# Performance work log

Hardware: AMD Instinct MI355X
Metric: run time of the kernel (lower is better)

## Reference

```python
import jax, jax.numpy as jnp
import numpy as np

K = 4            # number of expert kernels
TEMPERATURE = 30.0  # T_max, initial temperature
KS = 3
PAD = 1
STRIDE = 1


def setup_inputs() -> dict:
    key = jax.random.key(0)
    k1, k2, k3, k4, k5 = jax.random.split(key, 5)
    b, c_in, c_out, f, t, ctx = 32, 256, 256, 64, 64, 256
    x = jax.random.normal(k1, (b, c_in, f, t), dtype=jnp.float32)
    g = jax.random.normal(k2, (b, ctx), dtype=jnp.float32)
    # expert kernels: (k, out, in//groups, ks, ks), kaiming-normal-ish init
    fan_in = c_in * KS * KS
    weight = jax.random.normal(k3, (K, c_out, c_in, KS, KS), dtype=jnp.float32) * jnp.sqrt(2.0 / fan_in)
    # attention Dense: ctx -> k * att_groups (att_groups = 1)
    dense_w = jax.random.normal(k4, (ctx, K), dtype=jnp.float32) * jnp.sqrt(1.0 / ctx)
    dense_b = jnp.zeros((K,), dtype=jnp.float32)
    return {"x": x, "g": g, "weight": weight, "dense_w": dense_w, "dense_b": dense_b}


def reference(x, g, weight, dense_w, dense_b):
    b, c, f, t = x.shape
    k, c_out, c_in_pg, ks, _ = weight.shape
    # attention over k expert kernels, per batch element (att_groups = 1)
    logits = g @ dense_w + dense_b                      # (b, k)
    attention = jax.nn.softmax(logits / TEMPERATURE, axis=-1)
    # per-sample mixed kernel: (b, out, in, ks, ks)
    agg_w = jnp.einsum('bk,koihw->boihw', attention, weight)
    agg_w = agg_w.reshape(b * c_out, c_in_pg, ks, ks)
    # batched per-sample conv via feature_group_count = groups * b (groups = 1)
    xg = x.reshape(1, b * c, f, t)
    out = jax.lax.conv_general_dilated(
        xg, agg_w,
        window_strides=(STRIDE, STRIDE),
        padding=((PAD, PAD), (PAD, PAD)),
        lhs_dilation=(1, 1), rhs_dilation=(1, 1),
        dimension_numbers=('NCHW', 'OIHW', 'NCHW'),
        feature_group_count=b,
    )
    return out.reshape(b, c_out, out.shape[-2], out.shape[-1])
```

## Files before the change

kernel.cpp:

```cpp
#include <hip/hip_runtime.h>
#include <hip/hip_bf16.h>
#include <stdint.h>

#define BATCH 32
#define CIN   256
#define COUT  256
#define FH    64
#define FW    64
#define NK    4
#define CTX   256
#define TEMP  30.0f

typedef __attribute__((ext_vector_type(8))) short bf16x8;
typedef __attribute__((ext_vector_type(4))) float f32x4;

__device__ __forceinline__ unsigned short f2bf(float f) {
    union { float f; uint32_t u; } a; a.f = f;
    uint32_t r = a.u + 0x7fffu + ((a.u >> 16) & 1u);
    return (unsigned short)(r >> 16);
}

#define WMIX_OFF  1024
#define WMIX_BYTES (32u * 9u * 8u * 4u * 256u * 16u)
#define XP_OFF    (WMIX_OFF + WMIX_BYTES)

__global__ __launch_bounds__(256, 2) void mix_kernel(
        const float* __restrict__ weight,
        const float* __restrict__ g,
        const float* __restrict__ dw,
        const float* __restrict__ db,
        uint32_t* __restrict__ wmix) {
    __shared__ __align__(16) short S[2 * 8 * 2308];
    __shared__ float logit_s[8];
    __shared__ float att_s[8];

    const int t   = threadIdx.x;
    const int cog = blockIdx.x;
    const int bg  = blockIdx.y;
    const int co0 = cog * 8;
    const int b0  = bg * 2;
    const size_t EST = (size_t)COUT * CIN * 9;

    {
        const int p  = t >> 5;
        const int i0 = t & 31;
        const int nb = p >> 2, k = p & 3;
        const float* gp = g + (size_t)(b0 + nb) * CTX;
        float part = 0.f;
#pragma unroll
        for (int j = 0; j < 8; ++j) {
            const int i = i0 + j * 32;
            part += gp[i] * dw[i * NK + k];
        }
#pragma unroll
        for (int m = 1; m <= 16; m <<= 1) part += __shfl_xor(part, m);
        if (i0 == 0) logit_s[p] = part + db[k];
    }
    __syncthreads();
    if (t < 8) {
        const int nb = t >> 2;
        const float l0 = logit_s[nb * 4 + 0] * (1.f / TEMP);
        const float l1 = logit_s[nb * 4 + 1] * (1.f / TEMP);
        const float l2 = logit_s[nb * 4 + 2] * (1.f / TEMP);
        const float l3 = logit_s[nb * 4 + 3] * (1.f / TEMP);
        const float m  = fmaxf(fmaxf(l0, l1), fmaxf(l2, l3));
        const float e0 = expf(l0 - m), e1 = expf(l1 - m);
        const float e2 = expf(l2 - m), e3 = expf(l3 - m);
        const float s  = e0 + e1 + e2 + e3;
        const int   k  = t & 3;
        const float e  = (k == 0) ? e0 : (k == 1) ? e1 : (k == 2) ? e2 : e3;
        att_s[t] = e / s;
    }
    __syncthreads();

    float a[2][4];
#pragma unroll
    for (int nb = 0; nb < 2; ++nb)
#pragma unroll
        for (int k = 0; k < 4; ++k)
            a[nb][k] = att_s[nb * 4 + k];

    const int co_l  = t >> 5;
    const int inner = t & 31;
    const float* wbase = weight + (size_t)(co0 + co_l) * 2304;

#pragma unroll 2
    for (int i = 0; i < 18; ++i) {
        const int e4 = inner + 32 * i;
        float4 w[4];
#pragma unroll
        for (int k = 0; k < 4; ++k)
            w[k] = *(const float4*)(wbase + k * EST + (size_t)e4 * 4);
#pragma unroll
        for (int nb = 0; nb < 2; ++nb) {
            float mx = a[nb][0] * w[0].x + a[nb][1] * w[1].x + a[nb][2] * w[2].x + a[nb][3] * w[3].x;
            float my = a[nb][0] * w[0].y + a[nb][1] * w[1].y + a[nb][2] * w[2].y + a[nb][3] * w[3].y;
            float mz = a[nb][0] * w[0].z + a[nb][1] * w[1].z + a[nb][2] * w[2].z + a[nb][3] * w[3].z;
            float mw = a[nb][0] * w[0].w + a[nb][1] * w[1].w + a[nb][2] * w[2].w + a[nb][3] * w[3].w;
            uint32_t lo = (uint32_t)f2bf(mx) | ((uint32_t)f2bf(my) << 16);
            uint32_t hi = (uint32_t)f2bf(mz) | ((uint32_t)f2bf(mw) << 16);
            uint2* d = (uint2*)(S + ((nb * 8 + co_l) * 2308 + e4 * 4));
            *d = make_uint2(lo, hi);
        }
    }
    __syncthreads();

    const int co_w = t & 7;
    const int slot = t >> 3;
#pragma unroll 2
    for (int j = 0; j < 18; ++j) {
        const int GG  = j * 32 + slot;
        const int b_l = (GG >= 288) ? 1 : 0;
        const int rem = GG - b_l * 288;
        const int tap = rem >> 5;
        const int ch  = (rem >> 2) & 7;
        const int q   = rem & 3;
        const short* sp = S + (b_l * 8 + co_w) * 2308;
        const int ebase = (ch * 32 + q * 8) * 9 + tap;
        uint32_t d[4];
#pragma unroll
        for (int rp = 0; rp < 4; ++rp) {
            uint32_t lo = (uint16_t)sp[ebase + (2 * rp) * 9];
            uint32_t hi = (uint16_t)sp[ebase + (2 * rp + 1) * 9];
            d[rp] = lo | (hi << 16);
        }
        uint32_t* dst = wmix +
            ((((size_t)((b0 + b_l) * 9 + tap) * 8 + ch) * 4 + q) * 256 + co0 + co_w) * 4;
        *(uint4*)dst = make_uint4(d[0], d[1], d[2], d[3]);
    }
}

__global__ __launch_bounds__(256) void xpad_kernel(const float* __restrict__ x,
                                                   uint32_t* __restrict__ xp) {
    __shared__ uint32_t P[6 * 1088];
    const int t  = threadIdx.x;
    const int yg = blockIdx.x;
    const int ch = blockIdx.y;
    const int b  = blockIdx.z;

    for (int i = t; i < 6 * 1088; i += 256) P[i] = 0;
    __syncthreads();

    const int ci_l = t >> 3;
    const int col0 = (t & 7) * 8;
    const int q = ci_l >> 3, r = ci_l & 7;
    unsigned short* Ps = (unsigned short*)P;

#pragma unroll
    for (int yy = 0; yy < 6; ++yy) {
        const int y = yg * 6 + yy;
        if (y >= 1 && y <= 64) {
            const float* xr = x + (((size_t)(b * 256 + ch * 32 + ci_l) * 64) + (y - 1)) * 64 + col0;
            float4 v0 = *(const float4*)xr;
            float4 v1 = *(const float4*)(xr + 4);
            unsigned short bf[8];
            bf[0] = f2bf(v0.x); bf[1] = f2bf(v0.y); bf[2] = f2bf(v0.z); bf[3] = f2bf(v0.w);
            bf[4] = f2bf(v1.x); bf[5] = f2bf(v1.y); bf[6] = f2bf(v1.z); bf[7] = f2bf(v1.w);
#pragma unroll
            for (int j = 0; j < 8; ++j)
                Ps[yy * 2176 + (q * 68 + (col0 + j + 1)) * 8 + r] = bf[j];
        }
    }
    __syncthreads();

    const int qo = t >> 6, l = t & 63;
#pragma unroll
    for (int yy = 0; yy < 6; ++yy) {
        const int y = yg * 6 + yy;
        uint32_t* base = xp + (((((size_t)(b * 8 + ch) * 4 + qo) * 66) + y) * 68) * 4;
#pragma unroll
        for (int i = 0; i < 4; ++i)
            base[l + i * 64] = P[yy * 1088 + qo * 272 + l + i * 64];
        if (l < 16) base[l + 256] = P[yy * 1088 + qo * 272 + l + 256];
    }
}

__global__ __launch_bounds__(256, 2) void conv_mfma(
        const char* __restrict__ xp,
        const char* __restrict__ wmix,
        float* __restrict__ out) {
    __shared__ __align__(16) char As[2][3 * 4 * 2064];
    __shared__ __align__(16) char Bs[2][4 * 2192];

    const int tid  = threadIdx.x;
    const int lane = tid & 63;
    const int wv   = tid >> 6;
    const int wm   = wv & 1;
    const int wn   = wv >> 1;
    const int l4   = lane >> 4;
    const int m16  = lane & 15;

    const int bx  = blockIdx.x;
    const int wid = (bx & 7) * 256 + (bx >> 3);
    const int ptile = wid & 31;
    const int coT   = (wid >> 5) & 1;
    const int b     = wid >> 6;
    const int y0    = ptile * 2;

    const char* wmix_b = wmix + (size_t)b * 9 * 8 * 4 * 256 * 16;
    const char* xp_b   = xp + (size_t)b * 8 * 4 * 66 * 68 * 16;

    f32x4 acc[4][4];
#pragma unroll
    for (int i = 0; i < 4; ++i)
#pragma unroll
        for (int j = 0; j < 4; ++j)
            acc[i][j] = (f32x4){0.f, 0.f, 0.f, 0.f};

    const int aLane = l4 * 2064 + wm * 1024 + m16 * 16;
    const int bLane = l4 * 2192 + wn * 1088 + m16 * 16;

    auto stage = [&](char* Asb, char* Bsb, int p) {
        const int ch = p / 3, dy = p - ch * 3;
#pragma unroll
        for (int i = 0; i < 6; ++i) {
            const int s  = wv + i * 4;
            const int dx = s >> 3;
            const int q  = (s >> 1) & 3;
            const int h  = s & 1;
            const char* gsrc = wmix_b
                + ((size_t)((dy * 3 + dx) * 8 + ch) * 4 + q) * 4096
                + (coT * 128 + h * 64 + lane) * 16;
            char* ldst = Asb + dx * 8256 + q * 2064 + (h * 64 + lane) * 16;
            __builtin_amdgcn_global_load_lds(
                (const __attribute__((address_space(1))) void*)gsrc,
                (__attribute__((address_space(3))) void*)ldst, 16, 0, 0);
        }
        const int yb = y0 + dy;
        const char* gsrc = xp_b
            + (((size_t)ch * 4 + wv) * 66 + yb) * 1088 + lane * 16;
        char* ldst = Bsb + wv * 2192 + lane * 16;
        __builtin_amdgcn_global_load_lds(
            (const __attribute__((address_space(1))) void*)gsrc,
            (__attribute__((address_space(3))) void*)ldst, 16, 0, 0);
        __builtin_amdgcn_global_load_lds(
            (const __attribute__((address_space(1))) void*)(gsrc + 1024),
            (__attribute__((address_space(3))) void*)(ldst + 1024), 16, 0, 0);
        if (lane < 8)
            __builtin_amdgcn_global_load_lds(
                (const __attribute__((address_space(1))) void*)(gsrc + 2048),
                (__attribute__((address_space(3))) void*)(ldst + 2048), 16, 0, 0);
    };

    stage(As[0], Bs[0], 0);
    __syncthreads();

#pragma unroll 1
    for (int p = 0; p < 24; ++p) {
        const int cur = p & 1;
        if (p < 23) stage(As[cur ^ 1], Bs[cur ^ 1], p + 1);

        const char* Asc = As[cur];
        const char* Bsc = Bs[cur];
#pragma unroll
        for (int dx = 0; dx < 3; ++dx) {
            bf16x8 a[4], bb[4];
#pragma unroll
            for (int sm = 0; sm < 4; ++sm)
                a[sm] = *(const bf16x8*)(Asc + dx * 8256 + aLane + sm * 256);
#pragma unroll
            for (int sn = 0; sn < 4; ++sn)
                bb[sn] = *(const bf16x8*)(Bsc + bLane + dx * 16 + sn * 256);
            __builtin_amdgcn_s_setprio(1);
#pragma unroll
            for (int sm = 0; sm < 4; ++sm)
#pragma unroll
                for (int sn = 0; sn < 4; ++sn)
                    acc[sm][sn] = __builtin_amdgcn_mfma_f32_16x16x32_bf16(
                        a[sm], bb[sn], acc[sm][sn], 0, 0, 0);
            __builtin_amdgcn_s_setprio(0);
        }
        __syncthreads();
    }

    const int y = y0 + wn;
#pragma unroll
    for (int sm = 0; sm < 4; ++sm) {
#pragma unroll
        for (int sn = 0; sn < 4; ++sn) {
#pragma unroll
            for (int r = 0; r < 4; ++r) {
                const int co = coT * 128 + wm * 64 + sm * 16 + l4 * 4 + r;
                const int xx = sn * 16 + m16;
                out[(((size_t)b * COUT + co) * FH + y) * FW + xx] = acc[sm][sn][r];
            }
        }
    }
}

extern "C" void kernel_launch(void* const* d_in, const int* in_sizes, int n_in,
                              void* d_out, int out_size, void* d_ws, size_t ws_size,
                              hipStream_t stream) {
    const float* x       = (const float*)d_in[0];
    const float* g       = (const float*)d_in[1];
    const float* weight  = (const float*)d_in[2];
    const float* dense_w = (const float*)d_in[3];
    const float* dense_b = (const float*)d_in[4];
    float* out = (float*)d_out;

    uint32_t* wmix = (uint32_t*)((char*)d_ws + WMIX_OFF);
    uint32_t* xp   = (uint32_t*)((char*)d_ws + XP_OFF);

    mix_kernel<<<dim3(32, 16), 256, 0, stream>>>(weight, g, dense_w, dense_b, wmix);
    xpad_kernel<<<dim3(11, 8, BATCH), 256, 0, stream>>>(x, xp);
    conv_mfma<<<2048, 256, 0, stream>>>((const char*)xp, (const char*)wmix, out);
}
```

Measured before the change: 417.6 us.

## Merge prep kernels and read conv operands directly from global without LDS staging

Folds the weight-mixing and input-padding kernels into one launch whose blocks branch on block index, which saves a kernel launch and its serialization. The conv kernel drops its double-buffered LDS staging and loads MFMA operands straight from global memory into registers, relying on L1/L2 for reuse, and raises the occupancy hint to three blocks per CU. This removes LDS traffic and barriers, but each wave now fetches its operands separately and the global load latency is no longer hidden by explicit prefetch.

```diff
diff --git a/kernel.cpp b/kernel.cpp
--- a/kernel.cpp
+++ b/kernel.cpp
@@ -24,164 +24,166 @@
 #define WMIX_BYTES (32u * 9u * 8u * 4u * 256u * 16u)
 #define XP_OFF    (WMIX_OFF + WMIX_BYTES)
 
-__global__ __launch_bounds__(256, 2) void mix_kernel(
+__global__ __launch_bounds__(256, 2) void prep_kernel(
         const float* __restrict__ weight,
         const float* __restrict__ g,
         const float* __restrict__ dw,
         const float* __restrict__ db,
-        uint32_t* __restrict__ wmix) {
-    __shared__ __align__(16) short S[2 * 8 * 2308];
+        uint32_t* __restrict__ wmix,
+        const float* __restrict__ x,
+        uint32_t* __restrict__ xp) {
+    __shared__ __align__(16) char LDSU[73856];
     __shared__ float logit_s[8];
     __shared__ float att_s[8];
 
+    const int bid = blockIdx.x;
     const int t   = threadIdx.x;
-    const int cog = blockIdx.x;
-    const int bg  = blockIdx.y;
-    const int co0 = cog * 8;
-    const int b0  = bg * 2;
-    const size_t EST = (size_t)COUT * CIN * 9;
-
-    {
-        const int p  = t >> 5;
-        const int i0 = t & 31;
-        const int nb = p >> 2, k = p & 3;
-        const float* gp = g + (size_t)(b0 + nb) * CTX;
-        float part = 0.f;
-#pragma unroll
-        for (int j = 0; j < 8; ++j) {
-            const int i = i0 + j * 32;
-            part += gp[i] * dw[i * NK + k];
-        }
-#pragma unroll
-        for (int m = 1; m <= 16; m <<= 1) part += __shfl_xor(part, m);
-        if (i0 == 0) logit_s[p] = part + db[k];
+
+    if (bid < 512) {
+        short* S = (short*)LDSU;
+        const int cog = bid & 31;
+        const int bg  = bid >> 5;
+        const int co0 = cog * 8;
+        const int b0  = bg * 2;
+        const size_t EST = (size_t)COUT * CIN * 9;
+
+        {
+            const int p  = t >> 5;
+            const int i0 = t & 31;
+            const int nb = p >> 2, k = p & 3;
+            const float* gp = g + (size_t)(b0 + nb) * CTX;
+            float part = 0.f;
+#pragma unroll
+            for (int j = 0; j < 8; ++j) {
+                const int i = i0 + j * 32;
+                part += gp[i] * dw[i * NK + k];
+            }
+#pragma unroll
+            for (int m = 1; m <= 16; m <<= 1) part += __shfl_xor(part, m);
+            if (i0 == 0) logit_s[p] = part + db[k];
+        }
+        __syncthreads();
+        if (t < 8) {
+            const int nb = t >> 2;
+            const float l0 = logit_s[nb * 4 + 0] * (1.f / TEMP);
+            const float l1 = logit_s[nb * 4 + 1] * (1.f / TEMP);
+            const float l2 = logit_s[nb * 4 + 2] * (1.f / TEMP);
+            const float l3 = logit_s[nb * 4 + 3] * (1.f / TEMP);
+            const float m  = fmaxf(fmaxf(l0, l1), fmaxf(l2, l3));
+            const float e0 = expf(l0 - m), e1 = expf(l1 - m);
+            const float e2 = expf(l2 - m), e3 = expf(l3 - m);
+            const float s  = e0 + e1 + e2 + e3;
+            const int   k  = t & 3;
+            const float e  = (k == 0) ? e0 : (k == 1) ? e1 : (k == 2) ? e2 : e3;
+            att_s[t] = e / s;
+        }
+        __syncthreads();
+
+        float a[2][4];
+#pragma unroll
+        for (int nb = 0; nb < 2; ++nb)
+#pragma unroll
+            for (int k = 0; k < 4; ++k)
+                a[nb][k] = att_s[nb * 4 + k];
+
+        const int co_l  = t >> 5;
+        const int inner = t & 31;
+        const float* wbase = weight + (size_t)(co0 + co_l) * 2304;
+
+#pragma unroll 2
+        for (int i = 0; i < 18; ++i) {
+            const int e4 = inner + 32 * i;
+            float4 w[4];
+#pragma unroll
+            for (int k = 0; k < 4; ++k)
+                w[k] = *(const float4*)(wbase + k * EST + (size_t)e4 * 4);
+#pragma unroll
+            for (int nb = 0; nb < 2; ++nb) {
+                float mx = a[nb][0] * w[0].x + a[nb][1] * w[1].x + a[nb][2] * w[2].x + a[nb][3] * w[3].x;
+                float my = a[nb][0] * w[0].y + a[nb][1] * w[1].y + a[nb][2] * w[2].y + a[nb][3] * w[3].y;
+                float mz = a[nb][0] * w[0].z + a[nb][1] * w[1].z + a[nb][2] * w[2].z + a[nb][3] * w[3].z;
+                float mw = a[nb][0] * w[0].w + a[nb][1] * w[1].w + a[nb][2] * w[2].w + a[nb][3] * w[3].w;
+                uint32_t lo = (uint32_t)f2bf(mx) | ((uint32_t)f2bf(my) << 16);
+                uint32_t hi = (uint32_t)f2bf(mz) | ((uint32_t)f2bf(mw) << 16);
+                uint2* d = (uint2*)(S + ((nb * 8 + co_l) * 2308 + e4 * 4));
+                *d = make_uint2(lo, hi);
+            }
+        }
+        __syncthreads();
+
+        const int co_w = t & 7;
+        const int slot = t >> 3;
+#pragma unroll 2
+        for (int j = 0; j < 18; ++j) {
+            const int GG  = j * 32 + slot;
+            const int b_l = (GG >= 288) ? 1 : 0;
+            const int rem = GG - b_l * 288;
+            const int tap = rem >> 5;
+            const int ch  = (rem >> 2) & 7;
+            const int q   = rem & 3;
+            const short* sp = S + (b_l * 8 + co_w) * 2308;
+            const int ebase = (ch * 32 + q * 8) * 9 + tap;
+            uint32_t d[4];
+#pragma unroll
+            for (int rp = 0; rp < 4; ++rp) {
+                uint32_t lo = (uint16_t)sp[ebase + (2 * rp) * 9];
+                uint32_t hi = (uint16_t)sp[ebase + (2 * rp + 1) * 9];
+                d[rp] = lo | (hi << 16);
+            }
+            uint32_t* dst = wmix +
+                ((((size_t)((b0 + b_l) * 9 + tap) * 8 + ch) * 4 + q) * 256 + co0 + co_w) * 4;
+            *(uint4*)dst = make_uint4(d[0], d[1], d[2], d[3]);
+        }
+    } else {
+        uint32_t* P = (uint32_t*)LDSU;
+        const int idx = bid - 512;
+        const int yg  = idx % 11;
+        const int rem = idx / 11;
+        const int ch  = rem & 7;
+        const int b   = rem >> 3;
+
+        for (int i = t; i < 6 * 1088; i += 256) P[i] = 0;
+        __syncthreads();
+
+        const int ci_l = t >> 3;
+        const int col0 = (t & 7) * 8;
+        const int q = ci_l >> 3, r = ci_l & 7;
+        unsigned short* Ps = (unsigned short*)P;
+
+#pragma unroll
+        for (int yy = 0; yy < 6; ++yy) {
+            const int y = yg * 6 + yy;
+            if (y >= 1 && y <= 64) {
+                const float* xr = x + (((size_t)(b * 256 + ch * 32 + ci_l) * 64) + (y - 1)) * 64 + col0;
+                float4 v0 = *(const float4*)xr;
+                float4 v1 = *(const float4*)(xr + 4);
+                unsigned short bf[8];
+                bf[0] = f2bf(v0.x); bf[1] = f2bf(v0.y); bf[2] = f2bf(v0.z); bf[3] = f2bf(v0.w);
+                bf[4] = f2bf(v1.x); bf[5] = f2bf(v1.y); bf[6] = f2bf(v1.z); bf[7] = f2bf(v1.w);
+#pragma unroll
+                for (int j = 0; j < 8; ++j)
+                    Ps[yy * 2176 + (q * 68 + (col0 + j + 1)) * 8 + r] = bf[j];
+            }
+        }
+        __syncthreads();
+
+        const int qo = t >> 6, l = t & 63;
+#pragma unroll
+        for (int yy = 0; yy < 6; ++yy) {
+            const int y = yg * 6 + yy;
+            uint32_t* base = xp + (((((size_t)(b * 8 + ch) * 4 + qo) * 66) + y) * 68) * 4;
+#pragma unroll
+            for (int i = 0; i < 4; ++i)
+                base[l + i * 64] = P[yy * 1088 + qo * 272 + l + i * 64];
+            if (l < 16) base[l + 256] = P[yy * 1088 + qo * 272 + l + 256];
+        }
     }
-    __syncthreads();
-    if (t < 8) {
-        const int nb = t >> 2;
-        const float l0 = logit_s[nb * 4 + 0] * (1.f / TEMP);
-        const float l1 = logit_s[nb * 4 + 1] * (1.f / TEMP);
-        const float l2 = logit_s[nb * 4 + 2] * (1.f / TEMP);
-        const float l3 = logit_s[nb * 4 + 3] * (1.f / TEMP);
-        const float m  = fmaxf(fmaxf(l0, l1), fmaxf(l2, l3));
-        const float e0 = expf(l0 - m), e1 = expf(l1 - m);
-        const float e2 = expf(l2 - m), e3 = expf(l3 - m);
-        const float s  = e0 + e1 + e2 + e3;
-        const int   k  = t & 3;
-        const float e  = (k == 0) ? e0 : (k == 1) ? e1 : (k == 2) ? e2 : e3;
-        att_s[t] = e / s;
-    }
-    __syncthreads();
-
-    float a[2][4];
-#pragma unroll
-    for (int nb = 0; nb < 2; ++nb)
-#pragma unroll
-        for (int k = 0; k < 4; ++k)
-            a[nb][k] = att_s[nb * 4 + k];
-
-    const int co_l  = t >> 5;
-    const int inner = t & 31;
-    const float* wbase = weight + (size_t)(co0 + co_l) * 2304;
-
-#pragma unroll 2
-    for (int i = 0; i < 18; ++i) {
-        const int e4 = inner + 32 * i;
-        float4 w[4];
-#pragma unroll
-        for (int k = 0; k < 4; ++k)
-            w[k] = *(const float4*)(wbase + k * EST + (size_t)e4 * 4);
-#pragma unroll
-        for (int nb = 0; nb < 2; ++nb) {
-            float mx = a[nb][0] * w[0].x + a[nb][1] * w[1].x + a[nb][2] * w[2].x + a[nb][3] * w[3].x;
-            float my = a[nb][0] * w[0].y + a[nb][1] * w[1].y + a[nb][2] * w[2].y + a[nb][3] * w[3].y;
-            float mz = a[nb][0] * w[0].z + a[nb][1] * w[1].z + a[nb][2] * w[2].z + a[nb][3] * w[3].z;
-            float mw = a[nb][0] * w[0].w + a[nb][1] * w[1].w + a[nb][2] * w[2].w + a[nb][3] * w[3].w;
-            uint32_t lo = (uint32_t)f2bf(mx) | ((uint32_t)f2bf(my) << 16);
-            uint32_t hi = (uint32_t)f2bf(mz) | ((uint32_t)f2bf(mw) << 16);
-            uint2* d = (uint2*)(S + ((nb * 8 + co_l) * 2308 + e4 * 4));
-            *d = make_uint2(lo, hi);
-        }
-    }
-    __syncthreads();
-
-    const int co_w = t & 7;
-    const int slot = t >> 3;
-#pragma unroll 2
-    for (int j = 0; j < 18; ++j) {
-        const int GG  = j * 32 + slot;
-        const int b_l = (GG >= 288) ? 1 : 0;
-        const int rem = GG - b_l * 288;
-        const int tap = rem >> 5;
-        const int ch  = (rem >> 2) & 7;
-        const int q   = rem & 3;
-        const short* sp = S + (b_l * 8 + co_w) * 2308;
-        const int ebase = (ch * 32 + q * 8) * 9 + tap;
-        uint32_t d[4];
-#pragma unroll
-        for (int rp = 0; rp < 4; ++rp) {
-            uint32_t lo = (uint16_t)sp[ebase + (2 * rp) * 9];
-            uint32_t hi = (uint16_t)sp[ebase + (2 * rp + 1) * 9];
-            d[rp] = lo | (hi << 16);
-        }
-        uint32_t* dst = wmix +
-            ((((size_t)((b0 + b_l) * 9 + tap) * 8 + ch) * 4 + q) * 256 + co0 + co_w) * 4;
-        *(uint4*)dst = make_uint4(d[0], d[1], d[2], d[3]);
-    }
-}
-
-__global__ __launch_bounds__(256) void xpad_kernel(const float* __restrict__ x,
-                                                   uint32_t* __restrict__ xp) {
-    __shared__ uint32_t P[6 * 1088];
-    const int t  = threadIdx.x;
-    const int yg = blockIdx.x;
-    const int ch = blockIdx.y;
-    const int b  = blockIdx.z;
-
-    for (int i = t; i < 6 * 1088; i += 256) P[i] = 0;
-    __syncthreads();
-
-    const int ci_l = t >> 3;
-    const int col0 = (t & 7) * 8;
-    const int q = ci_l >> 3, r = ci_l & 7;
-    unsigned short* Ps = (unsigned short*)P;
-
-#pragma unroll
-    for (int yy = 0; yy < 6; ++yy) {
-        const int y = yg * 6 + yy;
-        if (y >= 1 && y <= 64) {
-            const float* xr = x + (((size_t)(b * 256 + ch * 32 + ci_l) * 64) + (y - 1)) * 64 + col0;
-            float4 v0 = *(const float4*)xr;
-            float4 v1 = *(const float4*)(xr + 4);
-            unsigned short bf[8];
-            bf[0] = f2bf(v0.x); bf[1] = f2bf(v0.y); bf[2] = f2bf(v0.z); bf[3] = f2bf(v0.w);
-            bf[4] = f2bf(v1.x); bf[5] = f2bf(v1.y); bf[6] = f2bf(v1.z); bf[7] = f2bf(v1.w);
-#pragma unroll
-            for (int j = 0; j < 8; ++j)
-                Ps[yy * 2176 + (q * 68 + (col0 + j + 1)) * 8 + r] = bf[j];
-        }
-    }
-    __syncthreads();
-
-    const int qo = t >> 6, l = t & 63;
-#pragma unroll
-    for (int yy = 0; yy < 6; ++yy) {
-        const int y = yg * 6 + yy;
-        uint32_t* base = xp + (((((size_t)(b * 8 + ch) * 4 + qo) * 66) + y) * 68) * 4;
-#pragma unroll
-        for (int i = 0; i < 4; ++i)
-            base[l + i * 64] = P[yy * 1088 + qo * 272 + l + i * 64];
-        if (l < 16) base[l + 256] = P[yy * 1088 + qo * 272 + l + 256];
-    }
-}
-
-__global__ __launch_bounds__(256, 2) void conv_mfma(
+}
+
+__global__ __launch_bounds__(256, 3) void conv_mfma(
         const char* __restrict__ xp,
         const char* __restrict__ wmix,
         float* __restrict__ out) {
-    __shared__ __align__(16) char As[2][3 * 4 * 2064];
-    __shared__ __align__(16) char Bs[2][4 * 2192];
-
     const int tid  = threadIdx.x;
     const int lane = tid & 63;
     const int wv   = tid >> 6;
@@ -207,73 +209,38 @@
         for (int j = 0; j < 4; ++j)
             acc[i][j] = (f32x4){0.f, 0.f, 0.f, 0.f};
 
-    const int aLane = l4 * 2064 + wm * 1024 + m16 * 16;
-    const int bLane = l4 * 2192 + wn * 1088 + m16 * 16;
-
-    auto stage = [&](char* Asb, char* Bsb, int p) {
-        const int ch = p / 3, dy = p - ch * 3;
-#pragma unroll
-        for (int i = 0; i < 6; ++i) {
-            const int s  = wv + i * 4;
-            const int dx = s >> 3;
-            const int q  = (s >> 1) & 3;
-            const int h  = s & 1;
-            const char* gsrc = wmix_b
-                + ((size_t)((dy * 3 + dx) * 8 + ch) * 4 + q) * 4096
-                + (coT * 128 + h * 64 + lane) * 16;
-            char* ldst = Asb + dx * 8256 + q * 2064 + (h * 64 + lane) * 16;
-            __builtin_amdgcn_global_load_lds(
-                (const __attribute__((address_space(1))) void*)gsrc,
-                (__attribute__((address_space(3))) void*)ldst, 16, 0, 0);
-        }
-        const int yb = y0 + dy;
-        const char* gsrc = xp_b
-            + (((size_t)ch * 4 + wv) * 66 + yb) * 1088 + lane * 16;
-        char* ldst = Bsb + wv * 2192 + lane * 16;
-        __builtin_amdgcn_global_load_lds(
-            (const __attribute__((address_space(1))) void*)gsrc,
-            (__attribute__((address_space(3))) void*)ldst, 16, 0, 0);
-        __builtin_amdgcn_global_load_lds(
-            (const __attribute__((address_space(1))) void*)(gsrc + 1024),
-            (__attribute__((address_space(3))) void*)(ldst + 1024), 16, 0, 0);
-        if (lane < 8)
-            __builtin_amdgcn_global_load_lds(
-                (const __attribute__((address_space(1))) void*)(gsrc + 2048),
-                (__attribute__((address_space(3))) void*)(ldst + 2048), 16, 0, 0);
-    };
-
-    stage(As[0], Bs[0], 0);
-    __syncthreads();
+    const char* Abase = wmix_b + (size_t)l4 * 4096
+                      + (size_t)(coT * 128 + wm * 64 + m16) * 16;
+    const int yout = y0 + wn;
 
 #pragma unroll 1
-    for (int p = 0; p < 24; ++p) {
-        const int cur = p & 1;
-        if (p < 23) stage(As[cur ^ 1], Bs[cur ^ 1], p + 1);
-
-        const char* Asc = As[cur];
-        const char* Bsc = Bs[cur];
-#pragma unroll
-        for (int dx = 0; dx < 3; ++dx) {
-            bf16x8 a[4], bb[4];
-#pragma unroll
-            for (int sm = 0; sm < 4; ++sm)
-                a[sm] = *(const bf16x8*)(Asc + dx * 8256 + aLane + sm * 256);
-#pragma unroll
-            for (int sn = 0; sn < 4; ++sn)
-                bb[sn] = *(const bf16x8*)(Bsc + bLane + dx * 16 + sn * 256);
-            __builtin_amdgcn_s_setprio(1);
-#pragma unroll
-            for (int sm = 0; sm < 4; ++sm)
+    for (int ch = 0; ch < 8; ++ch) {
+#pragma unroll
+        for (int dy = 0; dy < 3; ++dy) {
+            const char* Ap = Abase + (size_t)ch * 16384 + (size_t)(dy * 3) * 131072;
+            const char* Bp = xp_b
+                + (((size_t)(ch * 4 + l4)) * 66 + (yout + dy)) * 1088 + m16 * 16;
+#pragma unroll
+            for (int dx = 0; dx < 3; ++dx) {
+                bf16x8 a[4], bb[4];
+#pragma unroll
+                for (int sm = 0; sm < 4; ++sm)
+                    a[sm] = *(const bf16x8*)(Ap + dx * 131072 + sm * 256);
 #pragma unroll
                 for (int sn = 0; sn < 4; ++sn)
-                    acc[sm][sn] = __builtin_amdgcn_mfma_f32_16x16x32_bf16(
-                        a[sm], bb[sn], acc[sm][sn], 0, 0, 0);
-            __builtin_amdgcn_s_setprio(0);
-        }
-        __syncthreads();
+                    bb[sn] = *(const bf16x8*)(Bp + dx * 16 + sn * 256);
+                __builtin_amdgcn_s_setprio(1);
+#pragma unroll
+                for (int sm = 0; sm < 4; ++sm)
+#pragma unroll
+                    for (int sn = 0; sn < 4; ++sn)
+                        acc[sm][sn] = __builtin_amdgcn_mfma_f32_16x16x32_bf16(
+                            a[sm], bb[sn], acc[sm][sn], 0, 0, 0);
+                __builtin_amdgcn_s_setprio(0);
+            }
+        }
     }
 
-    const int y = y0 + wn;
 #pragma unroll
     for (int sm = 0; sm < 4; ++sm) {
 #pragma unroll
@@ -282,7 +249,7 @@
             for (int r = 0; r < 4; ++r) {
                 const int co = coT * 128 + wm * 64 + sm * 16 + l4 * 4 + r;
                 const int xx = sn * 16 + m16;
-                out[(((size_t)b * COUT + co) * FH + y) * FW + xx] = acc[sm][sn][r];
+                out[(((size_t)b * COUT + co) * FH + yout) * FW + xx] = acc[sm][sn][r];
             }
         }
     }
@@ -301,7 +268,6 @@
     uint32_t* wmix = (uint32_t*)((char*)d_ws + WMIX_OFF);
     uint32_t* xp   = (uint32_t*)((char*)d_ws + XP_OFF);
 
-    mix_kernel<<<dim3(32, 16), 256, 0, stream>>>(weight, g, dense_w, dense_b, wmix);
-    xpad_kernel<<<dim3(11, 8, BATCH), 256, 0, stream>>>(x, xp);
+    prep_kernel<<<3328, 256, 0, stream>>>(weight, g, dense_w, dense_b, wmix, x, xp);
     conv_mfma<<<2048, 256, 0, stream>>>((const char*)xp, (const char*)wmix, out);
 }
```

New measurement: 444.7 us. +6.5%, slower.

## Fuse prep kernels and single-buffer conv LDS for higher occupancy

Applied to the files above, without the earlier changes.

Merges the weight-mixing and input padding kernels into one launch, and shrinks mix blocks to four output channels so 1024 mix blocks run next to the 2816 pad blocks. In the conv kernel, it drops LDS double buffering and the padded strides and raises the launch bound to three blocks per CU. The goal is to hide load latency through more resident waves instead of software pipelining. The cost is two barriers per stage with no overlap of loads and MFMA inside a block, and the setprio hints are removed.

```diff
diff --git a/kernel.cpp b/kernel.cpp
--- a/kernel.cpp
+++ b/kernel.cpp
@@ -24,163 +24,168 @@
 #define WMIX_BYTES (32u * 9u * 8u * 4u * 256u * 16u)
 #define XP_OFF    (WMIX_OFF + WMIX_BYTES)
 
-__global__ __launch_bounds__(256, 2) void mix_kernel(
+__global__ __launch_bounds__(256) void prep_kernel(
         const float* __restrict__ weight,
         const float* __restrict__ g,
         const float* __restrict__ dw,
         const float* __restrict__ db,
-        uint32_t* __restrict__ wmix) {
-    __shared__ __align__(16) short S[2 * 8 * 2308];
+        uint32_t* __restrict__ wmix,
+        const float* __restrict__ x,
+        uint32_t* __restrict__ xp) {
+    __shared__ __align__(16) char LDSU[36928];
     __shared__ float logit_s[8];
     __shared__ float att_s[8];
 
+    const int bid = blockIdx.x;
     const int t   = threadIdx.x;
-    const int cog = blockIdx.x;
-    const int bg  = blockIdx.y;
-    const int co0 = cog * 8;
-    const int b0  = bg * 2;
-    const size_t EST = (size_t)COUT * CIN * 9;
-
-    {
-        const int p  = t >> 5;
-        const int i0 = t & 31;
-        const int nb = p >> 2, k = p & 3;
-        const float* gp = g + (size_t)(b0 + nb) * CTX;
-        float part = 0.f;
-#pragma unroll
-        for (int j = 0; j < 8; ++j) {
-            const int i = i0 + j * 32;
-            part += gp[i] * dw[i * NK + k];
-        }
-#pragma unroll
-        for (int m = 1; m <= 16; m <<= 1) part += __shfl_xor(part, m);
-        if (i0 == 0) logit_s[p] = part + db[k];
-    }
-    __syncthreads();
-    if (t < 8) {
-        const int nb = t >> 2;
-        const float l0 = logit_s[nb * 4 + 0] * (1.f / TEMP);
-        const float l1 = logit_s[nb * 4 + 1] * (1.f / TEMP);
-        const float l2 = logit_s[nb * 4 + 2] * (1.f / TEMP);
-        const float l3 = logit_s[nb * 4 + 3] * (1.f / TEMP);
-        const float m  = fmaxf(fmaxf(l0, l1), fmaxf(l2, l3));
-        const float e0 = expf(l0 - m), e1 = expf(l1 - m);
-        const float e2 = expf(l2 - m), e3 = expf(l3 - m);
-        const float s  = e0 + e1 + e2 + e3;
-        const int   k  = t & 3;
-        const float e  = (k == 0) ? e0 : (k == 1) ? e1 : (k == 2) ? e2 : e3;
-        att_s[t] = e / s;
-    }
-    __syncthreads();
-
-    float a[2][4];
-#pragma unroll
-    for (int nb = 0; nb < 2; ++nb)
-#pragma unroll
-        for (int k = 0; k < 4; ++k)
-            a[nb][k] = att_s[nb * 4 + k];
-
-    const int co_l  = t >> 5;
-    const int inner = t & 31;
-    const float* wbase = weight + (size_t)(co0 + co_l) * 2304;
-
-#pragma unroll 2
-    for (int i = 0; i < 18; ++i) {
-        const int e4 = inner + 32 * i;
-        float4 w[4];
-#pragma unroll
-        for (int k = 0; k < 4; ++k)
-            w[k] = *(const float4*)(wbase + k * EST + (size_t)e4 * 4);
-#pragma unroll
-        for (int nb = 0; nb < 2; ++nb) {
-            float mx = a[nb][0] * w[0].x + a[nb][1] * w[1].x + a[nb][2] * w[2].x + a[nb][3] * w[3].x;
-            float my = a[nb][0] * w[0].y + a[nb][1] * w[1].y + a[nb][2] * w[2].y + a[nb][3] * w[3].y;
-            float mz = a[nb][0] * w[0].z + a[nb][1] * w[1].z + a[nb][2] * w[2].z + a[nb][3] * w[3].z;
-            float mw = a[nb][0] * w[0].w + a[nb][1] * w[1].w + a[nb][2] * w[2].w + a[nb][3] * w[3].w;
-            uint32_t lo = (uint32_t)f2bf(mx) | ((uint32_t)f2bf(my) << 16);
-            uint32_t hi = (uint32_t)f2bf(mz) | ((uint32_t)f2bf(mw) << 16);
-            uint2* d = (uint2*)(S + ((nb * 8 + co_l) * 2308 + e4 * 4));
-            *d = make_uint2(lo, hi);
-        }
-    }
-    __syncthreads();
-
-    const int co_w = t & 7;
-    const int slot = t >> 3;
-#pragma unroll 2
-    for (int j = 0; j < 18; ++j) {
-        const int GG  = j * 32 + slot;
-        const int b_l = (GG >= 288) ? 1 : 0;
-        const int rem = GG - b_l * 288;
-        const int tap = rem >> 5;
-        const int ch  = (rem >> 2) & 7;
-        const int q   = rem & 3;
-        const short* sp = S + (b_l * 8 + co_w) * 2308;
-        const int ebase = (ch * 32 + q * 8) * 9 + tap;
-        uint32_t d[4];
-#pragma unroll
-        for (int rp = 0; rp < 4; ++rp) {
-            uint32_t lo = (uint16_t)sp[ebase + (2 * rp) * 9];
-            uint32_t hi = (uint16_t)sp[ebase + (2 * rp + 1) * 9];
-            d[rp] = lo | (hi << 16);
-        }
-        uint32_t* dst = wmix +
-            ((((size_t)((b0 + b_l) * 9 + tap) * 8 + ch) * 4 + q) * 256 + co0 + co_w) * 4;
-        *(uint4*)dst = make_uint4(d[0], d[1], d[2], d[3]);
+
+    if (bid < 2816) {
+        uint32_t* P = (uint32_t*)LDSU;
+        const int yg = bid % 11;
+        const int r2 = bid / 11;
+        const int ch = r2 & 7;
+        const int b  = r2 >> 3;
+
+        for (int i = t; i < 6 * 1088; i += 256) P[i] = 0;
+        __syncthreads();
+
+        const int ci_l = t >> 3;
+        const int col0 = (t & 7) * 8;
+        const int q = ci_l >> 3, r = ci_l & 7;
+        unsigned short* Ps = (unsigned short*)P;
+
+#pragma unroll
+        for (int yy = 0; yy < 6; ++yy) {
+            const int y = yg * 6 + yy;
+            if (y >= 1 && y <= 64) {
+                const float* xr = x + (((size_t)(b * 256 + ch * 32 + ci_l) * 64) + (y - 1)) * 64 + col0;
+                float4 v0 = *(const float4*)xr;
+                float4 v1 = *(const float4*)(xr + 4);
+                unsigned short bf[8];
+                bf[0] = f2bf(v0.x); bf[1] = f2bf(v0.y); bf[2] = f2bf(v0.z); bf[3] = f2bf(v0.w);
+                bf[4] = f2bf(v1.x); bf[5] = f2bf(v1.y); bf[6] = f2bf(v1.z); bf[7] = f2bf(v1.w);
+#pragma unroll
+                for (int j = 0; j < 8; ++j)
+                    Ps[yy * 2176 + (q * 68 + (col0 + j + 1)) * 8 + r] = bf[j];
+            }
+        }
+        __syncthreads();
+
+        const int qo = t >> 6, l = t & 63;
+#pragma unroll
+        for (int yy = 0; yy < 6; ++yy) {
+            const int y = yg * 6 + yy;
+            uint32_t* base = xp + (((((size_t)(b * 8 + ch) * 4 + qo) * 66) + y) * 68) * 4;
+#pragma unroll
+            for (int i = 0; i < 4; ++i)
+                base[l + i * 64] = P[yy * 1088 + qo * 272 + l + i * 64];
+            if (l < 16) base[l + 256] = P[yy * 1088 + qo * 272 + l + 256];
+        }
+    } else {
+        short* S = (short*)LDSU;
+        const int mb  = bid - 2816;
+        const int cog = mb & 63;
+        const int bg  = mb >> 6;
+        const int co0 = cog * 4;
+        const int b0  = bg * 2;
+        const size_t EST = (size_t)COUT * CIN * 9;
+
+        {
+            const int p  = t >> 5;
+            const int i0 = t & 31;
+            const int nb = p >> 2, k = p & 3;
+            const float* gp = g + (size_t)(b0 + nb) * CTX;
+            float part = 0.f;
+#pragma unroll
+            for (int j = 0; j < 8; ++j) {
+                const int i = i0 + j * 32;
+                part += gp[i] * dw[i * NK + k];
+            }
+#pragma unroll
+            for (int m = 1; m <= 16; m <<= 1) part += __shfl_xor(part, m);
+            if (i0 == 0) logit_s[p] = part + db[k];
+        }
+        __syncthreads();
+        if (t < 8) {
+            const int nb = t >> 2;
+            const float l0 = logit_s[nb * 4 + 0] * (1.f / TEMP);
+            const float l1 = logit_s[nb * 4 + 1] * (1.f / TEMP);
+            const float l2 = logit_s[nb * 4 + 2] * (1.f / TEMP);
+            const float l3 = logit_s[nb * 4 + 3] * (1.f / TEMP);
+            const float m  = fmaxf(fmaxf(l0, l1), fmaxf(l2, l3));
+            const float e0 = expf(l0 - m), e1 = expf(l1 - m);
+            const float e2 = expf(l2 - m), e3 = expf(l3 - m);
+            const float s  = e0 + e1 + e2 + e3;
+            const int   k  = t & 3;
+            const float e  = (k == 0) ? e0 : (k == 1) ? e1 : (k == 2) ? e2 : e3;
+            att_s[t] = e / s;
+        }
+        __syncthreads();
+
+        float a[2][4];
+#pragma unroll
+        for (int nb = 0; nb < 2; ++nb)
+#pragma unroll
+            for (int k = 0; k < 4; ++k)
+                a[nb][k] = att_s[nb * 4 + k];
+
+        const int co_l  = t >> 6;
+        const int inner = t & 63;
+        const float* wbase = weight + (size_t)(co0 + co_l) * 2304;
+
+#pragma unroll 3
+        for (int i = 0; i < 9; ++i) {
+            const int e4 = inner + 64 * i;
+            float4 w[4];
+#pragma unroll
+            for (int k = 0; k < 4; ++k)
+                w[k] = *(const float4*)(wbase + k * EST + (size_t)e4 * 4);
+#pragma unroll
+            for (int nb = 0; nb < 2; ++nb) {
+                float mx = a[nb][0] * w[0].x + a[nb][1] * w[1].x + a[nb][2] * w[2].x + a[nb][3] * w[3].x;
+                float my = a[nb][0] * w[0].y + a[nb][1] * w[1].y + a[nb][2] * w[2].y + a[nb][3] * w[3].y;
+                float mz = a[nb][0] * w[0].z + a[nb][1] * w[1].z + a[nb][2] * w[2].z + a[nb][3] * w[3].z;
+                float mw = a[nb][0] * w[0].w + a[nb][1] * w[1].w + a[nb][2] * w[2].w + a[nb][3] * w[3].w;
+                uint32_t lo = (uint32_t)f2bf(mx) | ((uint32_t)f2bf(my) << 16);
+                uint32_t hi = (uint32_t)f2bf(mz) | ((uint32_t)f2bf(mw) << 16);
+                uint2* d = (uint2*)(S + ((nb * 4 + co_l) * 2308 + e4 * 4));
+                *d = make_uint2(lo, hi);
+            }
+        }
+        __syncthreads();
+
+        const int co_w = t & 3;
+        const int slot = t >> 2;
+#pragma unroll 3
+        for (int j = 0; j < 9; ++j) {
+            const int GG  = j * 64 + slot;
+            const int b_l = (GG >= 288) ? 1 : 0;
+            const int rem = GG - b_l * 288;
+            const int tap = rem >> 5;
+            const int ch  = (rem >> 2) & 7;
+            const int q   = rem & 3;
+            const short* sp = S + (b_l * 4 + co_w) * 2308;
+            const int ebase = (ch * 32 + q * 8) * 9 + tap;
+            uint32_t d[4];
+#pragma unroll
+            for (int rp = 0; rp < 4; ++rp) {
+                uint32_t lo = (uint16_t)sp[ebase + (2 * rp) * 9];
+                uint32_t hi = (uint16_t)sp[ebase + (2 * rp + 1) * 9];
+                d[rp] = lo | (hi << 16);
+            }
+            uint32_t* dst = wmix +
+                ((((size_t)((b0 + b_l) * 9 + tap) * 8 + ch) * 4 + q) * 256 + co0 + co_w) * 4;
+            *(uint4*)dst = make_uint4(d[0], d[1], d[2], d[3]);
+        }
     }
 }
 
-__global__ __launch_bounds__(256) void xpad_kernel(const float* __restrict__ x,
-                                                   uint32_t* __restrict__ xp) {
-    __shared__ uint32_t P[6 * 1088];
-    const int t  = threadIdx.x;
-    const int yg = blockIdx.x;
-    const int ch = blockIdx.y;
-    const int b  = blockIdx.z;
-
-    for (int i = t; i < 6 * 1088; i += 256) P[i] = 0;
-    __syncthreads();
-
-    const int ci_l = t >> 3;
-    const int col0 = (t & 7) * 8;
-    const int q = ci_l >> 3, r = ci_l & 7;
-    unsigned short* Ps = (unsigned short*)P;
-
-#pragma unroll
-    for (int yy = 0; yy < 6; ++yy) {
-        const int y = yg * 6 + yy;
-        if (y >= 1 && y <= 64) {
-            const float* xr = x + (((size_t)(b * 256 + ch * 32 + ci_l) * 64) + (y - 1)) * 64 + col0;
-            float4 v0 = *(const float4*)xr;
-            float4 v1 = *(const float4*)(xr + 4);
-            unsigned short bf[8];
-            bf[0] = f2bf(v0.x); bf[1] = f2bf(v0.y); bf[2] = f2bf(v0.z); bf[3] = f2bf(v0.w);
-            bf[4] = f2bf(v1.x); bf[5] = f2bf(v1.y); bf[6] = f2bf(v1.z); bf[7] = f2bf(v1.w);
-#pragma unroll
-            for (int j = 0; j < 8; ++j)
-                Ps[yy * 2176 + (q * 68 + (col0 + j + 1)) * 8 + r] = bf[j];
-        }
-    }
-    __syncthreads();
-
-    const int qo = t >> 6, l = t & 63;
-#pragma unroll
-    for (int yy = 0; yy < 6; ++yy) {
-        const int y = yg * 6 + yy;
-        uint32_t* base = xp + (((((size_t)(b * 8 + ch) * 4 + qo) * 66) + y) * 68) * 4;
-#pragma unroll
-        for (int i = 0; i < 4; ++i)
-            base[l + i * 64] = P[yy * 1088 + qo * 272 + l + i * 64];
-        if (l < 16) base[l + 256] = P[yy * 1088 + qo * 272 + l + 256];
-    }
-}
-
-__global__ __launch_bounds__(256, 2) void conv_mfma(
+__global__ __launch_bounds__(256, 3) void conv_mfma(
         const char* __restrict__ xp,
         const char* __restrict__ wmix,
         float* __restrict__ out) {
-    __shared__ __align__(16) char As[2][3 * 4 * 2064];
-    __shared__ __align__(16) char Bs[2][4 * 2192];
+    __shared__ __align__(16) short As[3 * 4 * 128 * 8];
+    __shared__ __align__(16) short Bs[4 * 2 * 68 * 8];
 
     const int tid  = threadIdx.x;
     const int lane = tid & 63;
@@ -207,70 +212,63 @@
         for (int j = 0; j < 4; ++j)
             acc[i][j] = (f32x4){0.f, 0.f, 0.f, 0.f};
 
-    const int aLane = l4 * 2064 + wm * 1024 + m16 * 16;
-    const int bLane = l4 * 2192 + wn * 1088 + m16 * 16;
-
-    auto stage = [&](char* Asb, char* Bsb, int p) {
-        const int ch = p / 3, dy = p - ch * 3;
-#pragma unroll
-        for (int i = 0; i < 6; ++i) {
-            const int s  = wv + i * 4;
-            const int dx = s >> 3;
-            const int q  = (s >> 1) & 3;
-            const int h  = s & 1;
-            const char* gsrc = wmix_b
-                + ((size_t)((dy * 3 + dx) * 8 + ch) * 4 + q) * 4096
-                + (coT * 128 + h * 64 + lane) * 16;
-            char* ldst = Asb + dx * 8256 + q * 2064 + (h * 64 + lane) * 16;
-            __builtin_amdgcn_global_load_lds(
-                (const __attribute__((address_space(1))) void*)gsrc,
-                (__attribute__((address_space(3))) void*)ldst, 16, 0, 0);
-        }
-        const int yb = y0 + dy;
-        const char* gsrc = xp_b
-            + (((size_t)ch * 4 + wv) * 66 + yb) * 1088 + lane * 16;
-        char* ldst = Bsb + wv * 2192 + lane * 16;
-        __builtin_amdgcn_global_load_lds(
-            (const __attribute__((address_space(1))) void*)gsrc,
-            (__attribute__((address_space(3))) void*)ldst, 16, 0, 0);
-        __builtin_amdgcn_global_load_lds(
-            (const __attribute__((address_space(1))) void*)(gsrc + 1024),
-            (__attribute__((address_space(3))) void*)(ldst + 1024), 16, 0, 0);
-        if (lane < 8)
-            __builtin_amdgcn_global_load_lds(
-                (const __attribute__((address_space(1))) void*)(gsrc + 2048),
-                (__attribute__((address_space(3))) void*)(ldst + 2048), 16, 0, 0);
-    };
-
-    stage(As[0], Bs[0], 0);
-    __syncthreads();
+    const int aLane = l4 * 2048 + wm * 1024 + m16 * 16;
+    const int bLane = l4 * 2176 + wn * 1088 + m16 * 16;
 
 #pragma unroll 1
-    for (int p = 0; p < 24; ++p) {
-        const int cur = p & 1;
-        if (p < 23) stage(As[cur ^ 1], Bs[cur ^ 1], p + 1);
-
-        const char* Asc = As[cur];
-        const char* Bsc = Bs[cur];
-#pragma unroll
-        for (int dx = 0; dx < 3; ++dx) {
-            bf16x8 a[4], bb[4];
-#pragma unroll
-            for (int sm = 0; sm < 4; ++sm)
-                a[sm] = *(const bf16x8*)(Asc + dx * 8256 + aLane + sm * 256);
-#pragma unroll
-            for (int sn = 0; sn < 4; ++sn)
-                bb[sn] = *(const bf16x8*)(Bsc + bLane + dx * 16 + sn * 256);
-            __builtin_amdgcn_s_setprio(1);
-#pragma unroll
-            for (int sm = 0; sm < 4; ++sm)
+    for (int ch = 0; ch < 8; ++ch) {
+#pragma unroll 1
+        for (int dy = 0; dy < 3; ++dy) {
+            __syncthreads();
+#pragma unroll
+            for (int i = 0; i < 6; ++i) {
+                const int s  = wv + i * 4;
+                const int dx = s >> 3;
+                const int q  = (s >> 1) & 3;
+                const int h  = s & 1;
+                const char* gsrc = wmix_b
+                    + ((size_t)((dy * 3 + dx) * 8 + ch) * 4 + q) * 4096
+                    + (coT * 128 + h * 64 + lane) * 16;
+                char* ldst = (char*)As + ((dx * 4 + q) * 128 + h * 64 + lane) * 16;
+                __builtin_amdgcn_global_load_lds(
+                    (const __attribute__((address_space(1))) void*)gsrc,
+                    (__attribute__((address_space(3))) void*)ldst, 16, 0, 0);
+            }
+            {
+                const int yb = y0 + dy;
+                const char* gsrc = xp_b
+                    + (((size_t)ch * 4 + wv) * 66 + yb) * 1088 + lane * 16;
+                char* ldst = (char*)Bs + wv * 2176 + lane * 16;
+                __builtin_amdgcn_global_load_lds(
+                    (const __attribute__((address_space(1))) void*)gsrc,
+                    (__attribute__((address_space(3))) void*)ldst, 16, 0, 0);
+                __builtin_amdgcn_global_load_lds(
+                    (const __attribute__((address_space(1))) void*)(gsrc + 1024),
+                    (__attribute__((address_space(3))) void*)(ldst + 1024), 16, 0, 0);
+                if (lane < 8)
+                    __builtin_amdgcn_global_load_lds(
+                        (const __attribute__((address_space(1))) void*)(gsrc + 2048),
+                        (__attribute__((address_space(3))) void*)(ldst + 2048), 16, 0, 0);
+            }
+            __syncthreads();
+
+#pragma unroll
+            for (int dx = 0; dx < 3; ++dx) {
+                bf16x8 a[4], bb[4];
+#pragma unroll
+                for (int sm = 0; sm < 4; ++sm)
+                    a[sm] = *(const bf16x8*)((const char*)As + dx * 8192 + aLane + sm * 256);
 #pragma unroll
                 for (int sn = 0; sn < 4; ++sn)
-                    acc[sm][sn] = __builtin_amdgcn_mfma_f32_16x16x32_bf16(
-                        a[sm], bb[sn], acc[sm][sn], 0, 0, 0);
-            __builtin_amdgcn_s_setprio(0);
-        }
-        __syncthreads();
+                    bb[sn] = *(const bf16x8*)((const char*)Bs + bLane + dx * 16 + sn * 256);
+#pragma unroll
+                for (int sm = 0; sm < 4; ++sm)
+#pragma unroll
+                    for (int sn = 0; sn < 4; ++sn)
+                        acc[sm][sn] = __builtin_amdgcn_mfma_f32_16x16x32_bf16(
+                            a[sm], bb[sn], acc[sm][sn], 0, 0, 0);
+            }
+        }
     }
 
     const int y = y0 + wn;
@@ -301,7 +299,6 @@
     uint32_t* wmix = (uint32_t*)((char*)d_ws + WMIX_OFF);
     uint32_t* xp   = (uint32_t*)((char*)d_ws + XP_OFF);
 
-    mix_kernel<<<dim3(32, 16), 256, 0, stream>>>(weight, g, dense_w, dense_b, wmix);
-    xpad_kernel<<<dim3(11, 8, BATCH), 256, 0, stream>>>(x, xp);
+    prep_kernel<<<3840, 256, 0, stream>>>(weight, g, dense_w, dense_b, wmix, x, xp);
     conv_mfma<<<2048, 256, 0, stream>>>((const char*)xp, (const char*)wmix, out);
 }
```

Result: faster. 383.0 us (-8.3%).
